# Kernel optimization log

Hardware: AMD Instinct MI355X
Metric: run time of the kernel (lower is better)

Reference implementation:

```python
import jax, jax.numpy as jnp
import numpy as np

B, LQ, LS, S = 64, 64, 512, 512
NEG = -1e6


def mask_for_lengths(lengths, max_len, mask_right=True):
    pos = jnp.arange(max_len)
    if mask_right:
        m = pos[None, :] >= lengths[:, None]
    else:
        m = pos[None, :] < lengths[:, None]
    return jnp.where(m, jnp.float32(NEG), jnp.float32(0.0))


def setup_inputs() -> dict:
    key = jax.random.key(0)
    ks = jax.random.split(key, 12)
    f = lambda k, shp: jax.random.normal(k, shp, jnp.float32)
    sc = np.float32(1.0 / np.sqrt(S))
    return {
        "encoded_question": f(ks[0], (B, LQ, S)),
        "encoded_support": f(ks[1], (B, LS, S)),
        "question_length": jax.random.randint(ks[2], (B,), 1, LQ + 1),
        "support_length": jax.random.randint(ks[3], (B,), LS // 2, LS + 1),
        "correct_start": jax.random.randint(ks[4], (B,), 0, LS),
        "answer2question": jnp.arange(B),
        "is_eval": 1,
        "W_qa": f(ks[5], (S, 1)) * sc,
        "W_qsi": f(ks[6], (S, S)) * sc,
        "b_qsi": jnp.zeros((S,), jnp.float32),
        "W_qs": f(ks[7], (2 * S, S)) * sc,
        "W_ss": f(ks[8], (S, 1)) * sc,
        "W_qei": f(ks[9], (S, S)) * sc,
        "b_qei": jnp.zeros((S,), jnp.float32),
        "W_qe": f(ks[10], (3 * S, S)) * sc,
        "W_es": f(ks[11], (S, 1)) * sc,
    }


def reference(encoded_question, encoded_support, question_length, support_length,
              correct_start, answer2question, is_eval,
              W_qa, W_qsi, b_qsi, W_qs, W_ss, W_qei, b_qei, W_qe, W_es):
    # question attention pooling
    att = jnp.einsum('bqd,do->bq', encoded_question, W_qa)
    att = att + mask_for_lengths(question_length, LQ)
    w = jax.nn.softmax(att, axis=1)                                   # [B,LQ]
    q_state = jnp.einsum('bqd,bq->bd', encoded_question, w)           # [B,S]

    # start scoring
    start_input = jnp.concatenate(
        [q_state[:, None, :] * encoded_support, encoded_support], axis=2)  # [B,LS,2S]
    q_start_inter = q_state @ W_qsi + b_qsi                           # [B,S]
    q_start_state = start_input @ W_qs + q_start_inter[:, None, :]    # [B,LS,S]
    support_mask = mask_for_lengths(support_length, LS)
    start_scores = jnp.einsum('bld,do->bl', jax.nn.relu(q_start_state), W_ss)
    start_scores = start_scores + support_mask                        # [B,LS]
    predicted_start_pointer = jnp.argmax(start_scores, axis=1)        # [B]

    # eval path: start_pointer = predicted argmax
    start_pointer = predicted_start_pointer
    u_s = jnp.take_along_axis(encoded_support,
                              start_pointer[:, None, None], axis=1)[:, 0, :]  # [B,S]

    # end scoring
    end_input = jnp.concatenate(
        [encoded_support * u_s[:, None, :], start_input], axis=2)     # [B,LS,3S]
    q_end_inter = q_state @ W_qei + b_qei
    q_end_state = end_input @ W_qe + q_end_inter[:, None, :]          # [B,LS,S]
    end_scores = jnp.einsum('bld,do->bl', jax.nn.relu(q_end_state), W_es)
    end_scores = end_scores + support_mask
    # eval: mask positions left of start_pointer
    end_scores = end_scores + mask_for_lengths(start_pointer, LS, mask_right=False)
    predicted_end_pointer = jnp.argmax(end_scores, axis=1)

    return (start_scores, end_scores, predicted_start_pointer, predicted_end_pointer)
```

## Files before the change

kernel.cpp:

```cpp
#include <hip/hip_runtime.h>
#include <math.h>

constexpr int B_  = 64;
constexpr int LQ_ = 64;
constexpr int LS_ = 512;
constexpr int S_  = 512;
#define NEGV (-1e6f)
#define MARGIN 0.0625f

typedef __attribute__((ext_vector_type(8))) short bf16x8;
typedef __attribute__((ext_vector_type(4))) float f32x4;

__device__ inline unsigned short f2bf_rn(float x) {
    unsigned u = __builtin_bit_cast(unsigned, x);
    unsigned r = (u + 0x7FFFu + ((u >> 16) & 1u)) >> 16;
    return (unsigned short)r;
}

__global__ __launch_bounds__(512)
void prep_support_kernel(const float* __restrict__ support, short* __restrict__ Aprep)
{
    int bid = blockIdx.x;
    int b = bid >> 3, rg = bid & 7;
    int t = threadIdx.x;
    int r  = t & 63;
    int cg = t >> 6;
    int row  = rg * 64 + r;
    int rc2  = row >> 8;
    int rowp = row & 255;
    const float* src = support + ((size_t)(b * LS_ + row)) * S_;

    #pragma unroll
    for (int ii = 0; ii < 2; ++ii) {
        int i = cg * 2 + ii;
        #pragma unroll
        for (int kc = 0; kc < 4; ++kc) {
            int d0 = i * 32 + kc * 8;
            float4 f0 = *(const float4*)(src + d0);
            float4 f1 = *(const float4*)(src + d0 + 4);
            uint4 H;
            H.x = f2bf_rn(f0.x) | ((unsigned)f2bf_rn(f0.y) << 16);
            H.y = f2bf_rn(f0.z) | ((unsigned)f2bf_rn(f0.w) << 16);
            H.z = f2bf_rn(f1.x) | ((unsigned)f2bf_rn(f1.y) << 16);
            H.w = f2bf_rn(f1.z) | ((unsigned)f2bf_rn(f1.w) << 16);
            size_t off = ((size_t)(b * 2 + rc2) * 16 + i) * 8192 + kc * 2048 + rowp * 8;
            *(uint4*)&Aprep[off] = H;
        }
    }
}

__global__ __launch_bounds__(256)
void qpool_kernel(const float* __restrict__ eq, const int* __restrict__ qlen,
                  const float* __restrict__ W_qa, float* __restrict__ q_state)
{
    int b = blockIdx.x;
    int t = threadIdx.x;
    int wave = t >> 6, lane = t & 63;
    __shared__ float att[LQ_];
    __shared__ float wsm[LQ_];
    const float* eqb = eq + (size_t)b * LQ_ * S_;

    for (int k = 0; k < 16; ++k) {
        int q = wave + 4 * k;
        const float* row = eqb + q * S_;
        float s = 0.f;
        #pragma unroll
        for (int j = 0; j < S_ / 64; ++j)
            s = fmaf(row[lane + 64 * j], W_qa[lane + 64 * j], s);
        #pragma unroll
        for (int off = 32; off >= 1; off >>= 1)
            s += __shfl_xor(s, off);
        if (lane == 0) att[q] = s;
    }
    __syncthreads();

    if (wave == 0) {
        int L = qlen[b];
        float v = att[lane] + ((lane < L) ? 0.f : NEGV);
        float m = v;
        #pragma unroll
        for (int off = 32; off >= 1; off >>= 1)
            m = fmaxf(m, __shfl_xor(m, off));
        float e = expf(v - m);
        float sum = e;
        #pragma unroll
        for (int off = 32; off >= 1; off >>= 1)
            sum += __shfl_xor(sum, off);
        wsm[lane] = e / sum;
    }
    __syncthreads();

    for (int d = t; d < S_; d += 256) {
        float acc = 0.f;
        #pragma unroll 8
        for (int q = 0; q < LQ_; ++q)
            acc = fmaf(wsm[q], eqb[q * S_ + d], acc);
        q_state[b * S_ + d] = acc;
    }
}

__global__ __launch_bounds__(512)
void inter_kernel(const float* __restrict__ q_state,
                  const float* __restrict__ W_qsi, const float* __restrict__ b_qsi,
                  const float* __restrict__ W_qei, const float* __restrict__ b_qei,
                  float* __restrict__ qsi, float* __restrict__ qei)
{
    int b = blockIdx.x;
    const float* W  = blockIdx.y ? W_qei : W_qsi;
    const float* bi = blockIdx.y ? b_qei : b_qsi;
    float*       o  = blockIdx.y ? qei   : qsi;
    int t = threadIdx.x, lane = t & 63, w = t >> 6;
    __shared__ float qs[S_];
    __shared__ float red[8][S_];
    qs[t] = q_state[b * S_ + t];
    __syncthreads();

    float z[8];
    #pragma unroll
    for (int k = 0; k < 8; ++k) z[k] = 0.f;
    const int d0 = w * 64;
    #pragma unroll 4
    for (int dd = 0; dd < 64; ++dd) {
        int d = d0 + dd;
        float q = qs[d];
        const float* row = W + (size_t)d * S_ + lane;
        #pragma unroll
        for (int k = 0; k < 8; ++k)
            z[k] = fmaf(q, row[k * 64], z[k]);
    }
    #pragma unroll
    for (int k = 0; k < 8; ++k) red[w][k * 64 + lane] = z[k];
    __syncthreads();
    float acc = bi[t];
    #pragma unroll
    for (int ww = 0; ww < 8; ++ww) acc += red[ww][t];
    o[b * S_ + t] = acc;
}

template <int NT>
__global__ __launch_bounds__(512)
void prep_kernel(const float* __restrict__ W, const float* __restrict__ q_state,
                 const float* __restrict__ u_s, short* __restrict__ Wc)
{
    int bid = blockIdx.x;
    int i = bid >> 6, b = bid & 63;
    int col = threadIdx.x;
    __shared__ float scq[32], scu[32];
    if (col < 32) scq[col] = q_state[b * S_ + i * 32 + col];
    if (NT == 3 && col >= 32 && col < 64) scu[col - 32] = u_s[b * S_ + i * 32 + col - 32];
    __syncthreads();

    unsigned short h[32];
    #pragma unroll
    for (int d = 0; d < 32; ++d) {
        int D = i * 32 + d;
        float v;
        if (NT == 2)
            v = fmaf(scq[d], W[(size_t)D * S_ + col], W[(size_t)(S_ + D) * S_ + col]);
        else
            v = fmaf(scu[d], W[(size_t)D * S_ + col],
                fmaf(scq[d], W[(size_t)(S_ + D) * S_ + col], W[(size_t)(2 * S_ + D) * S_ + col]));
        h[d] = f2bf_rn(v);
    }
    size_t base = ((size_t)b * 16 + i) * 16384 + (size_t)col * 8;
    #pragma unroll
    for (int kc = 0; kc < 4; ++kc) {
        uint4 H;
        H.x = h[kc*8+0] | ((unsigned)h[kc*8+1] << 16);
        H.y = h[kc*8+2] | ((unsigned)h[kc*8+3] << 16);
        H.z = h[kc*8+4] | ((unsigned)h[kc*8+5] << 16);
        H.w = h[kc*8+6] | ((unsigned)h[kc*8+7] << 16);
        *(uint4*)&Wc[base + kc * 4096] = H;
    }
}

template <bool END>
__global__ __launch_bounds__(512, 2)
void score_kernel(const short* __restrict__ Aprep, const short* __restrict__ Wc,
                  const float* __restrict__ inter, const float* __restrict__ Wsmall,
                  const int* __restrict__ slen, const int* __restrict__ sp,
                  float* __restrict__ out)
{
    const int t = threadIdx.x;
    const int lane = t & 63, wid = t >> 6;
    const int wr = wid >> 2, wc = wid & 3;
    const int l15 = lane & 15, l4 = lane >> 4;

    int lid = blockIdx.x;
    int xcd = lid & 7, slot = lid >> 3;
    int b  = xcd * 8 + (slot >> 2);
    int rc = slot & 3;
    int rc2 = rc >> 1, hh = rc & 1;

    __shared__ __attribute__((aligned(16))) short As[2][4096];
    __shared__ __attribute__((aligned(16))) short Bs[2][16384];
    __shared__ float int_l[S_], wsm_l[S_];
    __shared__ float sm_red[128][4];

    int_l[t] = inter[b * S_ + t];
    wsm_l[t] = Wsmall[t];

    const char* Abase = (const char*)(Aprep + ((size_t)(b * 2 + rc2) * 16) * 8192);
    const char* Bbase = (const char*)(Wc    + ((size_t)b * 16) * 16384);

    f32x4 acc[4][8];
    #pragma unroll
    for (int r = 0; r < 4; ++r)
        #pragma unroll
        for (int c = 0; c < 8; ++c)
            acc[r][c] = (f32x4){0.f, 0.f, 0.f, 0.f};

    const int akc = t >> 7, ar = t & 127;

    auto stage = [&](int i, int buf) {
        const char* ga = Abase + (size_t)i * 16384 + akc * 4096 + hh * 2048 + ar * 16;
        char* la = (char*)As[buf] + t * 16;
        __builtin_amdgcn_global_load_lds(
            (const __attribute__((address_space(1))) void*)ga,
            (__attribute__((address_space(3))) void*)la, 16, 0, 0);
        const char* gb = Bbase + (size_t)i * 32768 + t * 16;
        char* lb = (char*)Bs[buf] + t * 16;
        #pragma unroll
        for (int q = 0; q < 4; ++q)
            __builtin_amdgcn_global_load_lds(
                (const __attribute__((address_space(1))) void*)(gb + q * 8192),
                (__attribute__((address_space(3))) void*)(lb + q * 8192), 16, 0, 0);
    };

    stage(0, 0);

    for (int i = 0; i < 16; ++i) {
        const int buf = i & 1;
        if (i + 1 < 16) {
            stage(i + 1, buf ^ 1);
            asm volatile("s_waitcnt vmcnt(5)" ::: "memory");
        } else {
            asm volatile("s_waitcnt vmcnt(0)" ::: "memory");
        }
        __builtin_amdgcn_s_barrier();

        bf16x8 ah[4];
        #pragma unroll
        for (int r = 0; r < 4; ++r) {
            int rowp = wr * 64 + r * 16 + l15;
            ah[r] = *(const bf16x8*)&As[buf][l4 * 1024 + rowp * 8];
        }
        #pragma unroll
        for (int c = 0; c < 8; ++c) {
            int col = wc * 128 + c * 16 + l15;
            bf16x8 bh = *(const bf16x8*)&Bs[buf][l4 * 4096 + col * 8];
            #pragma unroll
            for (int r = 0; r < 4; ++r)
                acc[r][c] = __builtin_amdgcn_mfma_f32_16x16x32_bf16(ah[r], bh, acc[r][c], 0, 0, 0);
        }
        asm volatile("s_waitcnt lgkmcnt(0)" ::: "memory");
        __builtin_amdgcn_s_barrier();
    }

    #pragma unroll
    for (int r = 0; r < 4; ++r) {
        #pragma unroll
        for (int jj = 0; jj < 4; ++jj) {
            float pr = 0.f;
            #pragma unroll
            for (int c = 0; c < 8; ++c) {
                int col = wc * 128 + c * 16 + l15;
                float v = acc[r][c][jj] + int_l[col];
                v = fmaxf(v, 0.f);
                pr = fmaf(v, wsm_l[col], pr);
            }
            pr += __shfl_xor(pr, 1);
            pr += __shfl_xor(pr, 2);
            pr += __shfl_xor(pr, 4);
            pr += __shfl_xor(pr, 8);
            if (l15 == 0) sm_red[wr * 64 + r * 16 + l4 * 4 + jj][wc] = pr;
        }
    }
    __syncthreads();
    if (t < 128) {
        int l = rc * 128 + t;
        float s = sm_red[t][0] + sm_red[t][1] + sm_red[t][2] + sm_red[t][3];
        if (l >= slen[b]) s += NEGV;
        if (END) { if (l < sp[b]) s += NEGV; }
        out[b * LS_ + l] = s;
    }
}

__device__ inline int select_cands(const float* s_l, int t, int lane, int w,
                                   float* wred, int* wcnt, int* cand)
{
    float v = s_l[t];
    #pragma unroll
    for (int off = 32; off >= 1; off >>= 1)
        v = fmaxf(v, __shfl_xor(v, off));
    if (lane == 0) wred[w] = v;
    __syncthreads();
    float m = wred[0];
    #pragma unroll
    for (int k = 1; k < 8; ++k) m = fmaxf(m, wred[k]);
    float th = m - MARGIN;
    bool flag = s_l[t] >= th;
    unsigned long long bal = __ballot(flag);
    int rank = __popcll(bal & ((1ull << lane) - 1ull));
    if (lane == 0) wcnt[w] = (int)__popcll(bal);
    __syncthreads();
    int off = 0, total = 0;
    #pragma unroll
    for (int k = 0; k < 8; ++k) { if (k < w) off += wcnt[k]; total += wcnt[k]; }
    if (flag) { int pos = off + rank; if (pos < 8) cand[pos] = t; }
    __syncthreads();
    return total < 8 ? total : 8;
}

template <bool END>
__global__ __launch_bounds__(512)
void rescue_fin_kernel(const float* __restrict__ support, const float* __restrict__ q_state,
                       const float* __restrict__ u_s_in, const float* __restrict__ Wbig,
                       const float* __restrict__ inter, const float* __restrict__ Wsmall,
                       const float* __restrict__ scores,
                       int* __restrict__ sp_ws, float* __restrict__ pred,
                       float* __restrict__ us_out)
{
    int b = blockIdx.x;
    int t = threadIdx.x, lane = t & 63, w = t >> 6;
    __shared__ float s_l[S_], qs_l[S_], us_l[S_], int_l[S_], wsm_l[S_];
    __shared__ float arow[8][S_];
    __shared__ float red[8][4][S_];
    __shared__ float wred[8];
    __shared__ int wcnt[8], cand[8];
    __shared__ float exact_v[8];
    __shared__ int best_sh;

    s_l[t]   = scores[b * S_ + t];
    qs_l[t]  = q_state[b * S_ + t];
    int_l[t] = inter[b * S_ + t];
    wsm_l[t] = Wsmall[t];
    if (END) us_l[t] = u_s_in[b * S_ + t];
    #pragma unroll
    for (int c = 0; c < 8; ++c) arow[c][t] = 0.f;
    __syncthreads();

    int cnt = select_cands(s_l, t, lane, w, wred, wcnt, cand);

    for (int c = 0; c < cnt; ++c)
        arow[c][t] = support[((size_t)(b * LS_ + cand[c])) * S_ + t];
    __syncthreads();

    const float* W1 = Wbig;
    const float* W2 = Wbig + (size_t)S_ * S_;
    const float* W3 = Wbig + (size_t)2 * S_ * S_;
    const int d0 = w * 64;

    for (int g = 0; g * 4 < cnt; ++g) {
        float z[4][8];
        #pragma unroll
        for (int cc = 0; cc < 4; ++cc)
            #pragma unroll
            for (int j = 0; j < 8; ++j) z[cc][j] = 0.f;

        #pragma unroll 2
        for (int dd = 0; dd < 64; ++dd) {
            int d = d0 + dd;
            float q = qs_l[d];
            float u = END ? us_l[d] : 0.f;
            float a[4], qa[4], ua[4];
            #pragma unroll
            for (int cc = 0; cc < 4; ++cc) {
                a[cc]  = arow[g * 4 + cc][d];
                qa[cc] = q * a[cc];
                if (END) ua[cc] = u * a[cc];
            }
            #pragma unroll
            for (int j = 0; j < 8; ++j) {
                int s = lane + 64 * j;
                float w1 = W1[(size_t)d * S_ + s];
                float w2 = W2[(size_t)d * S_ + s];
                if (END) {
                    float w3 = W3[(size_t)d * S_ + s];
                    #pragma unroll
                    for (int cc = 0; cc < 4; ++cc)
                        z[cc][j] = fmaf(ua[cc], w1, fmaf(qa[cc], w2, fmaf(a[cc], w3, z[cc][j])));
                } else {
                    #pragma unroll
                    for (int cc = 0; cc < 4; ++cc)
                        z[cc][j] = fmaf(qa[cc], w1, fmaf(a[cc], w2, z[cc][j]));
                }
            }
        }
        #pragma unroll
        for (int cc = 0; cc < 4; ++cc)
            #pragma unroll
            for (int j = 0; j < 8; ++j)
                red[w][cc][lane + 64 * j] = z[cc][j];
        __syncthreads();

        for (int cc = 0; cc < 4; ++cc) {
            float v = 0.f;
            #pragma unroll
            for (int ww = 0; ww < 8; ++ww) v += red[ww][cc][t];
            float p = fmaxf(v + int_l[t], 0.f) * wsm_l[t];
            #pragma unroll
            for (int off = 32; off >= 1; off >>= 1)
                p += __shfl_xor(p, off);
            if (lane == 0) wred[w] = p;
            __syncthreads();
            if (t == 0) {
                float e = ((wred[0] + wred[1]) + (wred[2] + wred[3])) +
                          ((wred[4] + wred[5]) + (wred[6] + wred[7]));
                exact_v[g * 4 + cc] = e;
            }
            __syncthreads();
        }
    }

    if (t == 0) {
        float bv = -INFINITY;
        int bi = cand[0];
        for (int c = 0; c < cnt; ++c) {
            float e = exact_v[c];
            if (e > bv) { bv = e; bi = cand[c]; }
        }
        best_sh = bi;
        pred[b] = (float)bi;
        if (!END) sp_ws[b] = bi;
    }
    __syncthreads();
    if (!END)
        us_out[b * S_ + t] = support[((size_t)(b * LS_ + best_sh)) * S_ + t];
}

extern "C" void kernel_launch(void* const* d_in, const int* in_sizes, int n_in,
                              void* d_out, int out_size, void* d_ws, size_t ws_size,
                              hipStream_t stream)
{
    const float* eq    = (const float*)d_in[0];
    const float* es    = (const float*)d_in[1];
    const int*   qlen  = (const int*)d_in[2];
    const int*   slen  = (const int*)d_in[3];
    const float* W_qa  = (const float*)d_in[7];
    const float* W_qsi = (const float*)d_in[8];
    const float* b_qsi = (const float*)d_in[9];
    const float* W_qs  = (const float*)d_in[10];
    const float* W_ss  = (const float*)d_in[11];
    const float* W_qei = (const float*)d_in[12];
    const float* b_qei = (const float*)d_in[13];
    const float* W_qe  = (const float*)d_in[14];
    const float* W_es  = (const float*)d_in[15];

    float* out          = (float*)d_out;
    float* start_scores = out;
    float* end_scores   = out + B_ * LS_;
    float* pred_start   = out + 2 * B_ * LS_;
    float* pred_end     = out + 2 * B_ * LS_ + B_;

    float* ws      = (float*)d_ws;
    float* q_state = ws;
    float* qsi     = ws + B_ * S_;
    float* qei     = ws + 2 * B_ * S_;
    float* u_s     = ws + 3 * B_ * S_;
    int*   sp_ws   = (int*)(ws + 4 * B_ * S_);
    short* Wc      = (short*)(ws + 4 * B_ * S_ + 64);
    short* Aprep   = Wc + (size_t)B_ * 16 * 16384;

    prep_support_kernel<<<512, 512, 0, stream>>>(es, Aprep);
    qpool_kernel<<<B_, 256, 0, stream>>>(eq, qlen, W_qa, q_state);
    inter_kernel<<<dim3(B_, 2), 512, 0, stream>>>(q_state, W_qsi, b_qsi, W_qei, b_qei, qsi, qei);

    prep_kernel<2><<<1024, 512, 0, stream>>>(W_qs, q_state, nullptr, Wc);
    score_kernel<false><<<256, 512, 0, stream>>>(Aprep, Wc, qsi, W_ss, slen, nullptr, start_scores);
    rescue_fin_kernel<false><<<B_, 512, 0, stream>>>(es, q_state, nullptr, W_qs, qsi, W_ss,
                                                     start_scores, sp_ws, pred_start, u_s);

    prep_kernel<3><<<1024, 512, 0, stream>>>(W_qe, q_state, u_s, Wc);
    score_kernel<true><<<256, 512, 0, stream>>>(Aprep, Wc, qei, W_es, slen, sp_ws, end_scores);
    rescue_fin_kernel<true><<<B_, 512, 0, stream>>>(es, q_state, u_s, W_qe, qei, W_es,
                                                    end_scores, nullptr, pred_end, nullptr);
}
```

Before: 187.4 us.

## Split rescue kernel into per-candidate blocks plus separate finalize kernel

The exact-recompute rescue step, which handled up to 8 argmax candidates in one block per batch, now runs as 8 blocks per batch, one candidate each, writing partial exact scores to workspace. A new finalize kernel reselects the candidates and picks the best from those partial scores. Batches with a single candidate now skip the recompute entirely. The aim is more parallelism across CUs for the weight-streaming GEMV. The cost is two extra kernel launches, duplicated candidate selection, and each block rereading the full weight matrices, where before one block's read was shared across four candidates.

After: 193.3 us. 3.2% more time.

```diff
diff --git a/kernel.cpp b/kernel.cpp
--- a/kernel.cpp
+++ b/kernel.cpp
@@ -314,36 +314,29 @@
 
 template <bool END>
 __global__ __launch_bounds__(512)
-void rescue_fin_kernel(const float* __restrict__ support, const float* __restrict__ q_state,
-                       const float* __restrict__ u_s_in, const float* __restrict__ Wbig,
-                       const float* __restrict__ inter, const float* __restrict__ Wsmall,
-                       const float* __restrict__ scores,
-                       int* __restrict__ sp_ws, float* __restrict__ pred,
-                       float* __restrict__ us_out)
-{
-    int b = blockIdx.x;
+void rescue_kernel(const float* __restrict__ support, const float* __restrict__ q_state,
+                   const float* __restrict__ u_s_in, const float* __restrict__ Wbig,
+                   const float* __restrict__ inter, const float* __restrict__ Wsmall,
+                   const float* __restrict__ scores, float* __restrict__ part)
+{
+    int bid = blockIdx.x;
+    int b = bid >> 3, cslot = bid & 7;
     int t = threadIdx.x, lane = t & 63, w = t >> 6;
-    __shared__ float s_l[S_], qs_l[S_], us_l[S_], int_l[S_], wsm_l[S_];
-    __shared__ float arow[8][S_];
-    __shared__ float red[8][4][S_];
+    __shared__ float s_l[S_], qs_l[S_], us_l[S_], arow_sh[S_];
+    __shared__ float red[8][S_];
     __shared__ float wred[8];
     __shared__ int wcnt[8], cand[8];
-    __shared__ float exact_v[8];
-    __shared__ int best_sh;
-
-    s_l[t]   = scores[b * S_ + t];
-    qs_l[t]  = q_state[b * S_ + t];
-    int_l[t] = inter[b * S_ + t];
-    wsm_l[t] = Wsmall[t];
+
+    s_l[t]  = scores[b * S_ + t];
+    qs_l[t] = q_state[b * S_ + t];
     if (END) us_l[t] = u_s_in[b * S_ + t];
-    #pragma unroll
-    for (int c = 0; c < 8; ++c) arow[c][t] = 0.f;
     __syncthreads();
 
     int cnt = select_cands(s_l, t, lane, w, wred, wcnt, cand);
-
-    for (int c = 0; c < cnt; ++c)
-        arow[c][t] = support[((size_t)(b * LS_ + cand[c])) * S_ + t];
+    if (cnt == 1 || cslot >= cnt) return;
+
+    int ci = cand[cslot];
+    arow_sh[t] = support[((size_t)(b * LS_ + ci)) * S_ + t];
     __syncthreads();
 
     const float* W1 = Wbig;
@@ -351,74 +344,72 @@
     const float* W3 = Wbig + (size_t)2 * S_ * S_;
     const int d0 = w * 64;
 
-    for (int g = 0; g * 4 < cnt; ++g) {
-        float z[4][8];
-        #pragma unroll
-        for (int cc = 0; cc < 4; ++cc)
-            #pragma unroll
-            for (int j = 0; j < 8; ++j) z[cc][j] = 0.f;
-
-        #pragma unroll 2
-        for (int dd = 0; dd < 64; ++dd) {
-            int d = d0 + dd;
-            float q = qs_l[d];
-            float u = END ? us_l[d] : 0.f;
-            float a[4], qa[4], ua[4];
-            #pragma unroll
-            for (int cc = 0; cc < 4; ++cc) {
-                a[cc]  = arow[g * 4 + cc][d];
-                qa[cc] = q * a[cc];
-                if (END) ua[cc] = u * a[cc];
+    float z[8];
+    #pragma unroll
+    for (int j = 0; j < 8; ++j) z[j] = 0.f;
+
+    #pragma unroll 2
+    for (int dd = 0; dd < 64; ++dd) {
+        int d = d0 + dd;
+        float a  = arow_sh[d];
+        float qa = qs_l[d] * a;
+        float ua = END ? us_l[d] * a : 0.f;
+        const float* r1 = W1 + (size_t)d * S_ + lane;
+        const float* r2 = W2 + (size_t)d * S_ + lane;
+        const float* r3 = W3 + (size_t)d * S_ + lane;
+        #pragma unroll
+        for (int j = 0; j < 8; ++j) {
+            if (END)
+                z[j] = fmaf(ua, r1[64 * j], fmaf(qa, r2[64 * j], fmaf(a, r3[64 * j], z[j])));
+            else
+                z[j] = fmaf(qa, r1[64 * j], fmaf(a, r2[64 * j], z[j]));
+        }
+    }
+    #pragma unroll
+    for (int j = 0; j < 8; ++j) red[w][lane + 64 * j] = z[j];
+    __syncthreads();
+
+    float v = 0.f;
+    #pragma unroll
+    for (int ww = 0; ww < 8; ++ww) v += red[ww][t];
+    float p = fmaxf(v + inter[b * S_ + t], 0.f) * Wsmall[t];
+    #pragma unroll
+    for (int off = 32; off >= 1; off >>= 1)
+        p += __shfl_xor(p, off);
+    if (lane == 0) wred[w] = p;
+    __syncthreads();
+    if (t == 0) {
+        float e = ((wred[0] + wred[1]) + (wred[2] + wred[3])) +
+                  ((wred[4] + wred[5]) + (wred[6] + wred[7]));
+        part[b * 8 + cslot] = e;
+    }
+}
+
+template <bool END>
+__global__ __launch_bounds__(512)
+void finalize_kernel(const float* __restrict__ scores, const float* __restrict__ part,
+                     const float* __restrict__ support, int* __restrict__ sp_ws,
+                     float* __restrict__ pred, float* __restrict__ us_out)
+{
+    int b = blockIdx.x;
+    int t = threadIdx.x, lane = t & 63, w = t >> 6;
+    __shared__ float s_l[S_];
+    __shared__ float wred[8];
+    __shared__ int wcnt[8], cand[8];
+    __shared__ int best_sh;
+
+    s_l[t] = scores[b * S_ + t];
+    __syncthreads();
+    int cnt = select_cands(s_l, t, lane, w, wred, wcnt, cand);
+
+    if (t == 0) {
+        int bi = cand[0];
+        if (cnt > 1) {
+            float bv = -INFINITY;
+            for (int c = 0; c < cnt; ++c) {
+                float e = part[b * 8 + c];
+                if (e > bv) { bv = e; bi = cand[c]; }
             }
-            #pragma unroll
-            for (int j = 0; j < 8; ++j) {
-                int s = lane + 64 * j;
-                float w1 = W1[(size_t)d * S_ + s];
-                float w2 = W2[(size_t)d * S_ + s];
-                if (END) {
-                    float w3 = W3[(size_t)d * S_ + s];
-                    #pragma unroll
-                    for (int cc = 0; cc < 4; ++cc)
-                        z[cc][j] = fmaf(ua[cc], w1, fmaf(qa[cc], w2, fmaf(a[cc], w3, z[cc][j])));
-                } else {
-                    #pragma unroll
-                    for (int cc = 0; cc < 4; ++cc)
-                        z[cc][j] = fmaf(qa[cc], w1, fmaf(a[cc], w2, z[cc][j]));
-                }
-            }
-        }
-        #pragma unroll
-        for (int cc = 0; cc < 4; ++cc)
-            #pragma unroll
-            for (int j = 0; j < 8; ++j)
-                red[w][cc][lane + 64 * j] = z[cc][j];
-        __syncthreads();
-
-        for (int cc = 0; cc < 4; ++cc) {
-            float v = 0.f;
-            #pragma unroll
-            for (int ww = 0; ww < 8; ++ww) v += red[ww][cc][t];
-            float p = fmaxf(v + int_l[t], 0.f) * wsm_l[t];
-            #pragma unroll
-            for (int off = 32; off >= 1; off >>= 1)
-                p += __shfl_xor(p, off);
-            if (lane == 0) wred[w] = p;
-            __syncthreads();
-            if (t == 0) {
-                float e = ((wred[0] + wred[1]) + (wred[2] + wred[3])) +
-                          ((wred[4] + wred[5]) + (wred[6] + wred[7]));
-                exact_v[g * 4 + cc] = e;
-            }
-            __syncthreads();
-        }
-    }
-
-    if (t == 0) {
-        float bv = -INFINITY;
-        int bi = cand[0];
-        for (int c = 0; c < cnt; ++c) {
-            float e = exact_v[c];
-            if (e > bv) { bv = e; bi = cand[c]; }
         }
         best_sh = bi;
         pred[b] = (float)bi;
@@ -458,8 +449,9 @@
     float* qsi     = ws + B_ * S_;
     float* qei     = ws + 2 * B_ * S_;
     float* u_s     = ws + 3 * B_ * S_;
-    int*   sp_ws   = (int*)(ws + 4 * B_ * S_);
-    short* Wc      = (short*)(ws + 4 * B_ * S_ + 64);
+    float* part    = ws + 4 * B_ * S_;
+    int*   sp_ws   = (int*)(ws + 4 * B_ * S_ + 512);
+    short* Wc      = (short*)(ws + 4 * B_ * S_ + 1024);
     short* Aprep   = Wc + (size_t)B_ * 16 * 16384;
 
     prep_support_kernel<<<512, 512, 0, stream>>>(es, Aprep);
@@ -468,11 +460,13 @@
 
     prep_kernel<2><<<1024, 512, 0, stream>>>(W_qs, q_state, nullptr, Wc);
     score_kernel<false><<<256, 512, 0, stream>>>(Aprep, Wc, qsi, W_ss, slen, nullptr, start_scores);
-    rescue_fin_kernel<false><<<B_, 512, 0, stream>>>(es, q_state, nullptr, W_qs, qsi, W_ss,
-                                                     start_scores, sp_ws, pred_start, u_s);
+    rescue_kernel<false><<<B_ * 8, 512, 0, stream>>>(es, q_state, nullptr, W_qs, qsi, W_ss,
+                                                     start_scores, part);
+    finalize_kernel<false><<<B_, 512, 0, stream>>>(start_scores, part, es, sp_ws, pred_start, u_s);
 
     prep_kernel<3><<<1024, 512, 0, stream>>>(W_qe, q_state, u_s, Wc);
     score_kernel<true><<<256, 512, 0, stream>>>(Aprep, Wc, qei, W_es, slen, sp_ws, end_scores);
-    rescue_fin_kernel<true><<<B_, 512, 0, stream>>>(es, q_state, u_s, W_qe, qei, W_es,
-                                                    end_scores, nullptr, pred_end, nullptr);
-}
+    rescue_kernel<true><<<B_ * 8, 512, 0, stream>>>(es, q_state, u_s, W_qe, qei, W_es,
+                                                    end_scores, part);
+    finalize_kernel<true><<<B_, 512, 0, stream>>>(end_scores, part, es, nullptr, pred_end, nullptr);
+}
```
